# Performance work log

Measured on AMD Instinct MI355X. Metric: run time of the kernel, lower is better.

## Reference

```python
import jax, jax.numpy as jnp
import numpy as np

BS, N, FEAT = 4, 4096, 64
LN_EPS = 1e-5


def setup_inputs() -> dict:
    key = jax.random.key(0)
    k1, k2, k3 = jax.random.split(key, 3)
    positions = jax.random.normal(k1, (BS, N, 3), dtype=jnp.float32)
    # nn.Linear(n_point, feature_dim): weight (FEAT, N), bias (FEAT,)
    W = jax.random.normal(k2, (FEAT, N), dtype=jnp.float32) * (1.0 / np.sqrt(N))
    b = jax.random.normal(k3, (FEAT,), dtype=jnp.float32) * 0.02
    gamma = jnp.ones((FEAT,), dtype=jnp.float32)
    beta = jnp.zeros((FEAT,), dtype=jnp.float32)
    return {"positions": positions, "W": W, "b": b, "gamma": gamma, "beta": beta}


def reference(positions, W, b, gamma, beta):
    # all-pairs squared distances: (bs, N, N)
    diff = positions[:, :, None, :] - positions[:, None, :, :]  # (bs,N,N,3)
    sq = jnp.sum(diff * diff, axis=-1)                          # (bs,N,N)
    # safe sqrt (diagonal is exactly 0)
    safe = jnp.where(sq > 0, sq, 1.0)
    dist = jnp.where(sq > 0, jnp.sqrt(safe), 0.0)               # (bs,N,N)
    # Linear(N -> FEAT)
    x = jnp.einsum('bnm,fm->bnf', dist, W) + b                  # (bs,N,FEAT)
    # LayerNorm over last dim (biased variance, eps=1e-5)
    mu = jnp.mean(x, axis=-1, keepdims=True)
    var = jnp.mean((x - mu) ** 2, axis=-1, keepdims=True)
    xn = (x - mu) / jnp.sqrt(var + LN_EPS) * gamma + beta
    # SiLU
    return xn * jax.nn.sigmoid(xn)
```

## Files before the change

### kernel.cpp

```cpp
#include <hip/hip_runtime.h>


typedef float f32x4 __attribute__((ext_vector_type(4)));
typedef __bf16 bf16x8 __attribute__((ext_vector_type(8)));

union BF8 { bf16x8 v; uint4 u; };

#define N_PTS 4096
#define FEATD 64
#define BK 256
#define NCH 16

__global__ void prep_kernel(const float* __restrict__ W,
                            const float* __restrict__ pos,
                            unsigned short* __restrict__ Wbt,
                            float* __restrict__ Pt) {
  int b = blockIdx.x, t = threadIdx.x;
  if (b < 128) {
    int gid = b * 256 + t;
    int f = gid >> 9, m8 = gid & 511;
    const float4* src = (const float4*)(W + (size_t)f * N_PTS + m8 * 8);
    float4 a = src[0], bb = src[1];
    BF8 o;
    o.v[0] = (__bf16)a.x;  o.v[1] = (__bf16)a.y;  o.v[2] = (__bf16)a.z;  o.v[3] = (__bf16)a.w;
    o.v[4] = (__bf16)bb.x; o.v[5] = (__bf16)bb.y; o.v[6] = (__bf16)bb.z; o.v[7] = (__bf16)bb.w;
    ((uint4*)Wbt)[(size_t)m8 * 64 + f] = o.u;
  } else {
    int bb = b - 128;
    int batch = bb >> 2, qtr = bb & 3;
    const float4* p4 = (const float4*)(pos + ((size_t)batch * N_PTS + qtr * 1024) * 3);
    float4 f0 = p4[t * 3 + 0], f1 = p4[t * 3 + 1], f2 = p4[t * 3 + 2];
    float4* Px = (float4*)(Pt + (size_t)(0 * 4 + batch) * N_PTS) + qtr * 256;
    float4* Py = (float4*)(Pt + (size_t)(1 * 4 + batch) * N_PTS) + qtr * 256;
    float4* Pz = (float4*)(Pt + (size_t)(2 * 4 + batch) * N_PTS) + qtr * 256;
    Px[t] = make_float4(f0.x, f0.w, f1.z, f2.y);
    Py[t] = make_float4(f0.y, f1.x, f1.w, f2.z);
    Pz[t] = make_float4(f0.z, f1.y, f2.x, f2.w);
  }
}

__device__ __forceinline__ void load_lds16(const void* g, void* l) {
  __builtin_amdgcn_global_load_lds(
      (const __attribute__((address_space(1))) void*)g,
      (__attribute__((address_space(3))) void*)l, 16, 0, 0);
}

__global__ __launch_bounds__(512, 4) void frp_kernel(
    const float* __restrict__ pos, const float* __restrict__ W,
    const float* __restrict__ bias, const float* __restrict__ gamma,
    const float* __restrict__ beta, const unsigned short* __restrict__ Wbt,
    const float* __restrict__ Pt, float* __restrict__ out) {
  __shared__ uint4 Wbuf[2][2048];

  const int tid = threadIdx.x;
  const int lane = tid & 63;
  const int wave = tid >> 6;
  const int fx = lane & 15;
  const int q = lane >> 4;

  const int batch = blockIdx.x >> 7;
  const int rb = (blockIdx.x & 127) * 32;
  const float* posB = pos + (size_t)batch * N_PTS * 3;
  const bool useWs = (Wbt != nullptr);

  const float* PxG = Pt + (size_t)(0 * 4 + batch) * N_PTS;
  const float* PyG = Pt + (size_t)(1 * 4 + batch) * N_PTS;
  const float* PzG = Pt + (size_t)(2 * 4 + batch) * N_PTS;

  float px0, py0, pz0, px1, py1, pz1;
  {
    int n0 = rb + fx;
    if (useWs) {
      px0 = PxG[n0];      py0 = PyG[n0];      pz0 = PzG[n0];
      px1 = PxG[n0 + 16]; py1 = PyG[n0 + 16]; pz1 = PzG[n0 + 16];
    } else {
      px0 = posB[n0 * 3];        py0 = posB[n0 * 3 + 1];        pz0 = posB[n0 * 3 + 2];
      px1 = posB[(n0 + 16) * 3]; py1 = posB[(n0 + 16) * 3 + 1]; pz1 = posB[(n0 + 16) * 3 + 2];
    }
  }

  auto stageW = [&](int c, int b) {
#pragma unroll
    for (int it = 0; it < 4; ++it) {
      int gi = it * 512 + tid;
      if (useWs) {
        load_lds16(Wbt + ((size_t)c * 2048 + gi) * 8, &Wbuf[b][gi]);
      } else {
        int g = gi >> 6, f = gi & 63;
        const float4* src = (const float4*)(W + (size_t)f * N_PTS + c * BK + g * 8);
        float4 a = src[0], b2 = src[1];
        BF8 o;
        o.v[0] = (__bf16)a.x;  o.v[1] = (__bf16)a.y;  o.v[2] = (__bf16)a.z;  o.v[3] = (__bf16)a.w;
        o.v[4] = (__bf16)b2.x; o.v[5] = (__bf16)b2.y; o.v[6] = (__bf16)b2.z; o.v[7] = (__bf16)b2.w;
        Wbuf[b][gi] = o.u;
      }
    }
  };

  f32x4 acc[2][4];
#pragma unroll
  for (int a = 0; a < 2; ++a)
#pragma unroll
    for (int t = 0; t < 4; ++t) acc[a][t] = (f32x4){0.f, 0.f, 0.f, 0.f};

  stageW(0, 0);
  __syncthreads();

  const int g8 = wave * 4 + q;

  for (int c = 0; c < NCH; ++c) {
    if (c + 1 < NCH) stageW(c + 1, (c + 1) & 1);
    const uint4* Wcur = Wbuf[c & 1];

    float kx[8], ky[8], kz[8];
    if (useWs) {
      const int m4 = c * 64 + g8 * 2;
      f32x4 xa = ((const f32x4*)PxG)[m4], xb = ((const f32x4*)PxG)[m4 + 1];
      f32x4 ya = ((const f32x4*)PyG)[m4], yb = ((const f32x4*)PyG)[m4 + 1];
      f32x4 za = ((const f32x4*)PzG)[m4], zb = ((const f32x4*)PzG)[m4 + 1];
#pragma unroll
      for (int j = 0; j < 4; ++j) {
        kx[j] = xa[j]; ky[j] = ya[j]; kz[j] = za[j];
        kx[4 + j] = xb[j]; ky[4 + j] = yb[j]; kz[4 + j] = zb[j];
      }
    } else {
      const float* pk = posB + ((size_t)c * BK + g8 * 8) * 3;
#pragma unroll
      for (int j = 0; j < 8; ++j) {
        kx[j] = pk[j * 3]; ky[j] = pk[j * 3 + 1]; kz[j] = pk[j * 3 + 2];
      }
    }

    bf16x8 af0, af1;
#pragma unroll
    for (int j = 0; j < 8; ++j) {
      float dx = kx[j] - px0, dy = ky[j] - py0, dz = kz[j] - pz0;
      af0[j] = (__bf16)__builtin_amdgcn_sqrtf(dx * dx + dy * dy + dz * dz);
      dx = kx[j] - px1; dy = ky[j] - py1; dz = kz[j] - pz1;
      af1[j] = (__bf16)__builtin_amdgcn_sqrtf(dx * dx + dy * dy + dz * dz);
    }

#pragma unroll
    for (int t = 0; t < 4; ++t) {
      BF8 bw;
      bw.u = Wcur[g8 * 64 + t * 16 + fx];
      acc[0][t] = __builtin_amdgcn_mfma_f32_16x16x32_bf16(af0, bw.v, acc[0][t], 0, 0, 0);
      acc[1][t] = __builtin_amdgcn_mfma_f32_16x16x32_bf16(af1, bw.v, acc[1][t], 0, 0, 0);
    }
    __syncthreads();
  }

  f32x4* mbv = (f32x4*)Wbuf;
  auto wr = [&](int rg) {
#pragma unroll
    for (int a = 0; a < 2; ++a)
#pragma unroll
      for (int t = 0; t < 4; ++t)
        mbv[rg * 512 + (a * 4 + t) * 64 + lane] = acc[a][t];
  };
  auto rd = [&](int rg) {
#pragma unroll
    for (int a = 0; a < 2; ++a)
#pragma unroll
      for (int t = 0; t < 4; ++t)
        acc[a][t] += mbv[rg * 512 + (a * 4 + t) * 64 + lane];
  };
  if (wave >= 4) wr(wave - 4);
  __syncthreads();
  if (wave < 4) rd(wave);
  __syncthreads();
  if (wave == 2 || wave == 3) wr(wave - 2);
  __syncthreads();
  if (wave < 2) rd(wave);
  __syncthreads();
  if (wave == 1) wr(0);
  __syncthreads();

  if (wave == 0) {
    rd(0);
    float bb[4], gg[4], be[4];
#pragma unroll
    for (int t = 0; t < 4; ++t) {
      bb[t] = bias[t * 16 + fx];
      gg[t] = gamma[t * 16 + fx];
      be[t] = beta[t * 16 + fx];
    }
    float* outB = out + ((size_t)batch * N_PTS + rb) * FEATD;
#pragma unroll
    for (int a = 0; a < 2; ++a) {
#pragma unroll
      for (int r = 0; r < 4; ++r) {
        float x[4], d[4];
#pragma unroll
        for (int t = 0; t < 4; ++t) x[t] = acc[a][t][r] + bb[t];
        float s = x[0] + x[1] + x[2] + x[3];
        s += __shfl_xor(s, 1); s += __shfl_xor(s, 2);
        s += __shfl_xor(s, 4); s += __shfl_xor(s, 8);
        float mu = s * (1.f / 64.f);
        float v = 0.f;
#pragma unroll
        for (int t = 0; t < 4; ++t) { d[t] = x[t] - mu; v += d[t] * d[t]; }
        v += __shfl_xor(v, 1); v += __shfl_xor(v, 2);
        v += __shfl_xor(v, 4); v += __shfl_xor(v, 8);
        float rstd = __builtin_amdgcn_rsqf(v * (1.f / 64.f) + 1e-5f);
        float* orow = outB + (a * 16 + q * 4 + r) * FEATD;
#pragma unroll
        for (int t = 0; t < 4; ++t) {
          float xn = d[t] * rstd * gg[t] + be[t];
          float y = xn * (1.f / (1.f + __expf(-xn)));
          orow[t * 16 + fx] = y;
        }
      }
    }
  }
}

extern "C" void kernel_launch(void* const* d_in, const int* in_sizes, int n_in,
                              void* d_out, int out_size, void* d_ws, size_t ws_size,
                              hipStream_t stream) {
  const float* pos   = (const float*)d_in[0];
  const float* W     = (const float*)d_in[1];
  const float* bias  = (const float*)d_in[2];
  const float* gamma = (const float*)d_in[3];
  const float* beta  = (const float*)d_in[4];
  float* out = (float*)d_out;

  const size_t wb_bytes = (size_t)FEATD * N_PTS * sizeof(unsigned short);
  const size_t pt_bytes = (size_t)3 * 4 * N_PTS * sizeof(float);
  int use_ws = (d_ws != nullptr && ws_size >= wb_bytes + pt_bytes);
  unsigned short* Wbt = use_ws ? (unsigned short*)d_ws : nullptr;
  float* Pt = use_ws ? (float*)((char*)d_ws + wb_bytes) : nullptr;

  if (use_ws) {
    prep_kernel<<<dim3(144), dim3(256), 0, stream>>>(W, pos, Wbt, Pt);
  }
  frp_kernel<<<dim3(512), dim3(512), 0, stream>>>(pos, W, bias, gamma, beta, Wbt, Pt, out);
}
```

Before: 95.34 us.

## Load bf16 W fragments directly from global, drop LDS staging and per-chunk barriers

Measured after the change: 362.1 us. 280% more time.

```diff
diff --git a/kernel.cpp b/kernel.cpp
--- a/kernel.cpp
+++ b/kernel.cpp
@@ -8,8 +8,6 @@
 
 #define N_PTS 4096
 #define FEATD 64
-#define BK 256
-#define NCH 16
 
 __global__ void prep_kernel(const float* __restrict__ W,
                             const float* __restrict__ pos,
@@ -39,18 +37,12 @@
   }
 }
 
-__device__ __forceinline__ void load_lds16(const void* g, void* l) {
-  __builtin_amdgcn_global_load_lds(
-      (const __attribute__((address_space(1))) void*)g,
-      (__attribute__((address_space(3))) void*)l, 16, 0, 0);
-}
-
-__global__ __launch_bounds__(512, 4) void frp_kernel(
+__global__ __launch_bounds__(512, 6) void frp_kernel(
     const float* __restrict__ pos, const float* __restrict__ W,
     const float* __restrict__ bias, const float* __restrict__ gamma,
     const float* __restrict__ beta, const unsigned short* __restrict__ Wbt,
     const float* __restrict__ Pt, float* __restrict__ out) {
-  __shared__ uint4 Wbuf[2][2048];
+  __shared__ f32x4 mbuf[4 * 512];
 
   const int tid = threadIdx.x;
   const int lane = tid & 63;
@@ -63,107 +55,111 @@
   const float* posB = pos + (size_t)batch * N_PTS * 3;
   const bool useWs = (Wbt != nullptr);
 
-  const float* PxG = Pt + (size_t)(0 * 4 + batch) * N_PTS;
-  const float* PyG = Pt + (size_t)(1 * 4 + batch) * N_PTS;
-  const float* PzG = Pt + (size_t)(2 * 4 + batch) * N_PTS;
-
-  float px0, py0, pz0, px1, py1, pz1;
-  {
-    int n0 = rb + fx;
-    if (useWs) {
-      px0 = PxG[n0];      py0 = PyG[n0];      pz0 = PzG[n0];
-      px1 = PxG[n0 + 16]; py1 = PyG[n0 + 16]; pz1 = PzG[n0 + 16];
-    } else {
-      px0 = posB[n0 * 3];        py0 = posB[n0 * 3 + 1];        pz0 = posB[n0 * 3 + 2];
-      px1 = posB[(n0 + 16) * 3]; py1 = posB[(n0 + 16) * 3 + 1]; pz1 = posB[(n0 + 16) * 3 + 2];
-    }
-  }
-
-  auto stageW = [&](int c, int b) {
-#pragma unroll
-    for (int it = 0; it < 4; ++it) {
-      int gi = it * 512 + tid;
-      if (useWs) {
-        load_lds16(Wbt + ((size_t)c * 2048 + gi) * 8, &Wbuf[b][gi]);
-      } else {
-        int g = gi >> 6, f = gi & 63;
-        const float4* src = (const float4*)(W + (size_t)f * N_PTS + c * BK + g * 8);
-        float4 a = src[0], b2 = src[1];
-        BF8 o;
-        o.v[0] = (__bf16)a.x;  o.v[1] = (__bf16)a.y;  o.v[2] = (__bf16)a.z;  o.v[3] = (__bf16)a.w;
-        o.v[4] = (__bf16)b2.x; o.v[5] = (__bf16)b2.y; o.v[6] = (__bf16)b2.z; o.v[7] = (__bf16)b2.w;
-        Wbuf[b][gi] = o.u;
-      }
-    }
-  };
-
   f32x4 acc[2][4];
 #pragma unroll
   for (int a = 0; a < 2; ++a)
 #pragma unroll
     for (int t = 0; t < 4; ++t) acc[a][t] = (f32x4){0.f, 0.f, 0.f, 0.f};
 
-  stageW(0, 0);
-  __syncthreads();
-
-  const int g8 = wave * 4 + q;
-
-  for (int c = 0; c < NCH; ++c) {
-    if (c + 1 < NCH) stageW(c + 1, (c + 1) & 1);
-    const uint4* Wcur = Wbuf[c & 1];
-
-    float kx[8], ky[8], kz[8];
-    if (useWs) {
-      const int m4 = c * 64 + g8 * 2;
+  const int G0 = wave * 4 + q;
+
+  if (useWs) {
+    const float* PxG = Pt + (size_t)(0 * 4 + batch) * N_PTS;
+    const float* PyG = Pt + (size_t)(1 * 4 + batch) * N_PTS;
+    const float* PzG = Pt + (size_t)(2 * 4 + batch) * N_PTS;
+    const uint4* Wq = (const uint4*)Wbt;
+
+    const int n0 = rb + fx;
+    const float px0 = PxG[n0],      py0 = PyG[n0],      pz0 = PzG[n0];
+    const float px1 = PxG[n0 + 16], py1 = PyG[n0 + 16], pz1 = PzG[n0 + 16];
+
+#pragma unroll 2
+    for (int c = 0; c < 16; ++c) {
+      const int G = c * 32 + G0;
+      const int m4 = G * 2;
       f32x4 xa = ((const f32x4*)PxG)[m4], xb = ((const f32x4*)PxG)[m4 + 1];
       f32x4 ya = ((const f32x4*)PyG)[m4], yb = ((const f32x4*)PyG)[m4 + 1];
       f32x4 za = ((const f32x4*)PzG)[m4], zb = ((const f32x4*)PzG)[m4 + 1];
-#pragma unroll
-      for (int j = 0; j < 4; ++j) {
-        kx[j] = xa[j]; ky[j] = ya[j]; kz[j] = za[j];
-        kx[4 + j] = xb[j]; ky[4 + j] = yb[j]; kz[4 + j] = zb[j];
-      }
-    } else {
-      const float* pk = posB + ((size_t)c * BK + g8 * 8) * 3;
+      const uint4* wg = Wq + (size_t)G * 64 + fx;
+      uint4 w0 = wg[0], w1 = wg[16], w2 = wg[32], w3 = wg[48];
+
+      bf16x8 af0, af1;
+      {
+        f32x4 dx = xa - px0, dy = ya - py0, dz = za - pz0;
+        f32x4 sq = dx * dx + dy * dy + dz * dz;
+#pragma unroll
+        for (int j = 0; j < 4; ++j) af0[j] = (__bf16)__builtin_amdgcn_sqrtf(sq[j]);
+        dx = xb - px0; dy = yb - py0; dz = zb - pz0;
+        sq = dx * dx + dy * dy + dz * dz;
+#pragma unroll
+        for (int j = 0; j < 4; ++j) af0[4 + j] = (__bf16)__builtin_amdgcn_sqrtf(sq[j]);
+        dx = xa - px1; dy = ya - py1; dz = za - pz1;
+        sq = dx * dx + dy * dy + dz * dz;
+#pragma unroll
+        for (int j = 0; j < 4; ++j) af1[j] = (__bf16)__builtin_amdgcn_sqrtf(sq[j]);
+        dx = xb - px1; dy = yb - py1; dz = zb - pz1;
+        sq = dx * dx + dy * dy + dz * dz;
+#pragma unroll
+        for (int j = 0; j < 4; ++j) af1[4 + j] = (__bf16)__builtin_amdgcn_sqrtf(sq[j]);
+      }
+      BF8 b0, b1, b2, b3;
+      b0.u = w0; b1.u = w1; b2.u = w2; b3.u = w3;
+      acc[0][0] = __builtin_amdgcn_mfma_f32_16x16x32_bf16(af0, b0.v, acc[0][0], 0, 0, 0);
+      acc[1][0] = __builtin_amdgcn_mfma_f32_16x16x32_bf16(af1, b0.v, acc[1][0], 0, 0, 0);
+      acc[0][1] = __builtin_amdgcn_mfma_f32_16x16x32_bf16(af0, b1.v, acc[0][1], 0, 0, 0);
+      acc[1][1] = __builtin_amdgcn_mfma_f32_16x16x32_bf16(af1, b1.v, acc[1][1], 0, 0, 0);
+      acc[0][2] = __builtin_amdgcn_mfma_f32_16x16x32_bf16(af0, b2.v, acc[0][2], 0, 0, 0);
+      acc[1][2] = __builtin_amdgcn_mfma_f32_16x16x32_bf16(af1, b2.v, acc[1][2], 0, 0, 0);
+      acc[0][3] = __builtin_amdgcn_mfma_f32_16x16x32_bf16(af0, b3.v, acc[0][3], 0, 0, 0);
+      acc[1][3] = __builtin_amdgcn_mfma_f32_16x16x32_bf16(af1, b3.v, acc[1][3], 0, 0, 0);
+    }
+  } else {
+    const int n0 = rb + fx;
+    const float px0 = posB[n0 * 3], py0 = posB[n0 * 3 + 1], pz0 = posB[n0 * 3 + 2];
+    const float px1 = posB[(n0 + 16) * 3], py1 = posB[(n0 + 16) * 3 + 1],
+                pz1 = posB[(n0 + 16) * 3 + 2];
+    for (int c = 0; c < 16; ++c) {
+      const int G = c * 32 + G0;
+      float kx[8], ky[8], kz[8];
 #pragma unroll
       for (int j = 0; j < 8; ++j) {
-        kx[j] = pk[j * 3]; ky[j] = pk[j * 3 + 1]; kz[j] = pk[j * 3 + 2];
-      }
-    }
-
-    bf16x8 af0, af1;
-#pragma unroll
-    for (int j = 0; j < 8; ++j) {
-      float dx = kx[j] - px0, dy = ky[j] - py0, dz = kz[j] - pz0;
-      af0[j] = (__bf16)__builtin_amdgcn_sqrtf(dx * dx + dy * dy + dz * dz);
-      dx = kx[j] - px1; dy = ky[j] - py1; dz = kz[j] - pz1;
-      af1[j] = (__bf16)__builtin_amdgcn_sqrtf(dx * dx + dy * dy + dz * dz);
-    }
-
-#pragma unroll
-    for (int t = 0; t < 4; ++t) {
-      BF8 bw;
-      bw.u = Wcur[g8 * 64 + t * 16 + fx];
-      acc[0][t] = __builtin_amdgcn_mfma_f32_16x16x32_bf16(af0, bw.v, acc[0][t], 0, 0, 0);
-      acc[1][t] = __builtin_amdgcn_mfma_f32_16x16x32_bf16(af1, bw.v, acc[1][t], 0, 0, 0);
-    }
-    __syncthreads();
-  }
-
-  f32x4* mbv = (f32x4*)Wbuf;
+        const float* pk = posB + ((size_t)G * 8 + j) * 3;
+        kx[j] = pk[0]; ky[j] = pk[1]; kz[j] = pk[2];
+      }
+      bf16x8 af0, af1;
+#pragma unroll
+      for (int j = 0; j < 8; ++j) {
+        float dx = kx[j] - px0, dy = ky[j] - py0, dz = kz[j] - pz0;
+        af0[j] = (__bf16)__builtin_amdgcn_sqrtf(dx * dx + dy * dy + dz * dz);
+        dx = kx[j] - px1; dy = ky[j] - py1; dz = kz[j] - pz1;
+        af1[j] = (__bf16)__builtin_amdgcn_sqrtf(dx * dx + dy * dy + dz * dz);
+      }
+#pragma unroll
+      for (int t = 0; t < 4; ++t) {
+        int f = t * 16 + fx;
+        const float* wr = W + (size_t)f * N_PTS + G * 8;
+        BF8 bw;
+#pragma unroll
+        for (int j = 0; j < 8; ++j) bw.v[j] = (__bf16)wr[j];
+        acc[0][t] = __builtin_amdgcn_mfma_f32_16x16x32_bf16(af0, bw.v, acc[0][t], 0, 0, 0);
+        acc[1][t] = __builtin_amdgcn_mfma_f32_16x16x32_bf16(af1, bw.v, acc[1][t], 0, 0, 0);
+      }
+    }
+  }
+
   auto wr = [&](int rg) {
 #pragma unroll
     for (int a = 0; a < 2; ++a)
 #pragma unroll
       for (int t = 0; t < 4; ++t)
-        mbv[rg * 512 + (a * 4 + t) * 64 + lane] = acc[a][t];
+        mbuf[rg * 512 + (a * 4 + t) * 64 + lane] = acc[a][t];
   };
   auto rd = [&](int rg) {
 #pragma unroll
     for (int a = 0; a < 2; ++a)
 #pragma unroll
       for (int t = 0; t < 4; ++t)
-        acc[a][t] += mbv[rg * 512 + (a * 4 + t) * 64 + lane];
+        acc[a][t] += mbuf[rg * 512 + (a * 4 + t) * 64 + lane];
   };
   if (wave >= 4) wr(wave - 4);
   __syncthreads();
```
